# Kernel optimization log

Measured on AMD Instinct MI355X. Metric: run time of the kernel, lower is better.

Reference implementation:

```python
import jax, jax.numpy as jnp
import numpy as np

D_MODEL = 1024
N_HEAD = 16
HEAD_DIM = D_MODEL // N_HEAD

def setup_inputs() -> dict:
    key = jax.random.key(0)
    k1, k2, k3 = jax.random.split(key, 3)
    x = jax.random.normal(k1, (2, 2048, D_MODEL), dtype=jnp.float32)
    # torch Linear weights: [out_features, in_features]; scale like default init
    w_in = jax.random.normal(k2, (3 * D_MODEL, D_MODEL), dtype=jnp.float32) * (1.0 / np.sqrt(D_MODEL))
    w_out = jax.random.normal(k3, (D_MODEL, D_MODEL), dtype=jnp.float32) * (1.0 / np.sqrt(D_MODEL))
    return {"x": x, "w_in": w_in, "w_out": w_out}

def reference(x, w_in, w_out):
    B, T, D = x.shape
    qkv = jnp.einsum('btd,ed->bte', x, w_in)  # [B,T,3D]
    q, k, v = jnp.split(qkv, 3, axis=2)
    def heads(t):
        return t.reshape(B, T, N_HEAD, HEAD_DIM).transpose(0, 2, 1, 3)  # [B,H,T,hd]
    q, k, v = heads(q), heads(k), heads(v)
    att = jnp.einsum('bhqd,bhkd->bhqk', q, k) / np.sqrt(HEAD_DIM).astype(np.float32)
    # NOTE: original uses .tril() (zeroing, NOT -inf) before softmax — faithful reproduction
    causal = jnp.tril(jnp.ones((T, T), dtype=bool))
    att = jnp.where(causal, att, 0.0)
    att = jax.nn.softmax(att, axis=-1)
    out = jnp.einsum('bhqk,bhkd->bhqd', att, v)
    out = out.transpose(0, 2, 1, 3).reshape(B, T, D)
    return jnp.einsum('btd,ed->bte', out, w_out)
```

## Files before the change

### kernel.cpp

```cpp
#include <hip/hip_runtime.h>
#include <hip/hip_bf16.h>
#include <stdint.h>

#define TSEQ   2048
#define DMODEL 1024
#define NHEAD  16
#define HDIM   64

typedef __attribute__((ext_vector_type(8))) __bf16 bf16x8;
typedef __attribute__((ext_vector_type(4))) float f32x4;
typedef __attribute__((ext_vector_type(8))) unsigned short u16x8;

#define SC_LOG2E 0.18033688011112042f

#if __has_builtin(__builtin_amdgcn_exp2f)
#define EXP2F(x) __builtin_amdgcn_exp2f(x)
#else
#define EXP2F(x) __expf(0.6931471805599453f * (x))
#endif

__device__ __forceinline__ unsigned short f2bf(float f) {
    __hip_bfloat16 h = __float2bfloat16(f);
    return __builtin_bit_cast(unsigned short, h);
}
__device__ __forceinline__ float bf2f(unsigned short u) {
    union { unsigned int i; float f; } v;
    v.i = ((unsigned int)u) << 16;
    return v.f;
}

__device__ __forceinline__ void gld_lds16(const void* g, void* s) {
    __builtin_amdgcn_global_load_lds(
        (__attribute__((address_space(1))) void*)(void*)g,
        (__attribute__((address_space(3))) void*)s, 16, 0, 0);
}

#define NX4  (4096 * 1024 / 4)
#define NWI4 (3072 * 1024 / 4)
#define NWO4 (1024 * 1024 / 4)
__global__ void cast3_kernel(const float* __restrict__ x,
                             const float* __restrict__ wi,
                             const float* __restrict__ wo,
                             unsigned short* __restrict__ ox,
                             unsigned short* __restrict__ owi,
                             unsigned short* __restrict__ owo) {
    int i = blockIdx.x * blockDim.x + threadIdx.x;
    const float* s;
    unsigned short* d;
    int off;
    if (i < NX4)              { s = x;  d = ox;  off = i; }
    else if (i < NX4 + NWI4)  { s = wi; d = owi; off = i - NX4; }
    else                      { s = wo; d = owo; off = i - NX4 - NWI4; }
    float4 v = ((const float4*)s)[off];
    ushort4 u;
    u.x = f2bf(v.x); u.y = f2bf(v.y); u.z = f2bf(v.z); u.w = f2bf(v.w);
    ((ushort4*)d)[off] = u;
}

template<bool STORE_F32>
__global__ __launch_bounds__(256, 2)
void gemm_bt(const unsigned short* __restrict__ A,
             const unsigned short* __restrict__ B,
             void* __restrict__ C, int M, int N, int K) {
    (void)M;
    __shared__ unsigned short As[128 * 32];
    __shared__ unsigned short Bs[128 * 32];
    const int tid = threadIdx.x;
    const int nb = N >> 7;
    const int bm = blockIdx.x / nb;
    const int bn = blockIdx.x % nb;
    const int w  = tid >> 6, l = tid & 63;
    const int wr = w >> 1,  wc = w & 1;
    const int lr = l & 15,  lg = l >> 4;

    f32x4 acc[4][4] = {};

    const unsigned short* Ab = A + (size_t)bm * 128 * K;
    const unsigned short* Bb = B + (size_t)bn * 128 * K;

    const int c0 = tid, c1 = tid + 256;
    const int ar0 = c0 >> 2, ak0 = (c0 & 3) * 8;
    const int ar1 = c1 >> 2, ak1 = (c1 & 3) * 8;

    for (int kt = 0; kt < K; kt += 32) {
        __syncthreads();
        gld_lds16(Ab + (size_t)ar0 * K + kt + ak0, As + c0 * 8);
        gld_lds16(Ab + (size_t)ar1 * K + kt + ak1, As + c1 * 8);
        gld_lds16(Bb + (size_t)ar0 * K + kt + ak0, Bs + c0 * 8);
        gld_lds16(Bb + (size_t)ar1 * K + kt + ak1, Bs + c1 * 8);
        __syncthreads();

        bf16x8 af[4], bfr[4];
#pragma unroll
        for (int i = 0; i < 4; i++)
            af[i] = *(const bf16x8*)(As + (wr * 64 + i * 16 + lr) * 32 + lg * 8);
#pragma unroll
        for (int i = 0; i < 4; i++)
            bfr[i] = *(const bf16x8*)(Bs + (wc * 64 + i * 16 + lr) * 32 + lg * 8);
#pragma unroll
        for (int mi = 0; mi < 4; mi++)
#pragma unroll
            for (int ni = 0; ni < 4; ni++)
                acc[mi][ni] = __builtin_amdgcn_mfma_f32_16x16x32_bf16(
                    af[mi], bfr[ni], acc[mi][ni], 0, 0, 0);
    }

    const int row0 = bm * 128 + wr * 64;
    const int col0 = bn * 128 + wc * 64;
    const float qsc = (!STORE_F32 && bn < 8) ? SC_LOG2E : 1.0f;
#pragma unroll
    for (int mi = 0; mi < 4; mi++)
#pragma unroll
        for (int ni = 0; ni < 4; ni++)
#pragma unroll
            for (int r = 0; r < 4; r++) {
                const int row = row0 + mi * 16 + lg * 4 + r;
                const int col = col0 + ni * 16 + lr;
                if (STORE_F32)
                    ((float*)C)[(size_t)row * N + col] = acc[mi][ni][r];
                else
                    ((unsigned short*)C)[(size_t)row * N + col] =
                        f2bf(acc[mi][ni][r] * qsc);
            }
}

__global__ __launch_bounds__(256)
void vtran_kernel(const unsigned short* __restrict__ qkv,
                  unsigned short* __restrict__ vtg,
                  float* __restrict__ ts) {
    __shared__ unsigned short T[64][72];
    const int bid = blockIdx.x;
    const int kb_ = bid & 31;
    const int bh  = bid >> 5;
    const int b = bh >> 4, h = bh & 15;
    const int tid = threadIdx.x;

    const int r = tid >> 2, cq = (tid & 3) * 16;
    const unsigned short* src =
        qkv + ((size_t)(b * TSEQ + kb_ * 64 + r)) * 3072 + 2048 + h * 64 + cq;
    u16x8 v0 = *(const u16x8*)src;
    u16x8 v1 = *(const u16x8*)(src + 8);
#pragma unroll
    for (int i = 0; i < 8; i++) T[r][cq + i] = v0[i];
#pragma unroll
    for (int i = 0; i < 8; i++) T[r][cq + 8 + i] = v1[i];
    __syncthreads();

    const int d = tid >> 2, kq = (tid & 3) * 16;
    u16x8 o0, o1;
#pragma unroll
    for (int i = 0; i < 8; i++) o0[i] = T[kq + i][d];
#pragma unroll
    for (int i = 0; i < 8; i++) o1[i] = T[kq + 8 + i][d];
    unsigned short* dst = vtg + ((size_t)bh * 64 + d) * TSEQ + kb_ * 64 + kq;
    *(u16x8*)dst = o0;
    *(u16x8*)(dst + 8) = o1;

    float ps = 0.f;
#pragma unroll
    for (int i = 0; i < 8; i++) ps += bf2f(o0[i]) + bf2f(o1[i]);
    ps += __shfl_xor(ps, 1);
    ps += __shfl_xor(ps, 2);
    if ((tid & 3) == 0)
        ts[((size_t)bh * 32 + kb_) * 64 + d] = ps;
}

__global__ void vsuf2_kernel(const float* __restrict__ ts,
                             float* __restrict__ tsuf) {
    const int bh = blockIdx.x, d = threadIdx.x;
    float acc = 0.f;
    for (int t = 31; t >= 0; --t) {
        tsuf[((size_t)bh * 32 + t) * 64 + d] = acc;
        acc += ts[((size_t)bh * 32 + t) * 64 + d];
    }
}

__global__ __launch_bounds__(256, 2)
void attn_kernel(const unsigned short* __restrict__ qkv,
                 const unsigned short* __restrict__ vtg,
                 const float* __restrict__ tsuf,
                 unsigned short* __restrict__ out) {
    __shared__ __attribute__((aligned(16))) unsigned short Ks[2][4096];
    __shared__ __attribute__((aligned(16))) unsigned short Vs[2][4096];
    __shared__ __attribute__((aligned(16))) unsigned short Pl[4][32 * 72];

    const int tid = threadIdx.x;
    const int w = tid >> 6, l = tid & 63, lr = l & 15, lg = l >> 4;
    const int bid = blockIdx.x;
    const int j  = bid >> 5;
    const int s  = (j < 8) ? j : 23 - j;
    const int bh = (bid & 7) * 4 + ((bid >> 3) & 3);
    const int b = bh >> 4, h = bh & 15;
    const int strip  = 2 * s + ((w < 2) ? 1 : 0);
    const int lastkt = strip;
    const int ntiles = 2 * s + 2;
    const size_t rowbase = (size_t)b * TSEQ;
    const int qrow0 = strip * 64 + (w & 1) * 32;

    bf16x8 qf[2][2];
#pragma unroll
    for (int mi = 0; mi < 2; mi++) {
        const unsigned short* qp =
            qkv + (rowbase + qrow0 + mi * 16 + lr) * 3072 + h * 64 + lg * 8;
        qf[mi][0] = *(const bf16x8*)qp;
        qf[mi][1] = *(const bf16x8*)(qp + 32);
    }

    bf16x8 onesf;
#pragma unroll
    for (int i = 0; i < 8; i++) onesf[i] = (__bf16)1.0f;

    const unsigned short* ksrc[2];
    const unsigned short* vsrc[2];
#pragma unroll
    for (int jj = 0; jj < 2; jj++) {
        const int d = tid + jj * 256;
        const int fr = (d >> 7) * 16 + (d & 15);
        const int cc = ((d >> 6) & 1) * 32 + ((d & 63) >> 4) * 8;
        ksrc[jj] = qkv + (rowbase + fr) * 3072 + 1024 + h * 64 + cc;
        vsrc[jj] = vtg + ((size_t)bh * 64 + fr) * TSEQ + cc;
    }

#define STAGE(kt_, bufi) do {                                      \
        const size_t ko_ = (size_t)(kt_) * 64 * 3072;              \
        const int vo_ = (kt_) * 64;                                \
        gld_lds16(ksrc[0] + ko_, &Ks[bufi][tid * 8]);              \
        gld_lds16(ksrc[1] + ko_, &Ks[bufi][tid * 8 + 2048]);       \
        gld_lds16(vsrc[0] + vo_, &Vs[bufi][tid * 8]);              \
        gld_lds16(vsrc[1] + vo_, &Vs[bufi][tid * 8 + 2048]);       \
    } while (0)

    f32x4 o[2][4] = {};
    f32x4 rs[2] = {};
    unsigned short* pw = &Pl[w][0];

    STAGE(0, 0);
    __syncthreads();

    int cur = 0;
    for (int kt = 0; kt < ntiles; ++kt) {
        if (kt + 1 < ntiles) STAGE(kt + 1, cur ^ 1);

        if (kt <= lastkt) {
            const unsigned short* kc = Ks[cur];
            const unsigned short* vc = Vs[cur];

            bf16x8 kb[4][2];
#pragma unroll
            for (int f = 0; f < 4; f++) {
                kb[f][0] = *(const bf16x8*)(kc + ((f * 2 + 0) * 64 + l) * 8);
                kb[f][1] = *(const bf16x8*)(kc + ((f * 2 + 1) * 64 + l) * 8);
            }

            float pvv[2][4][4];
            __builtin_amdgcn_s_setprio(1);
#pragma unroll
            for (int mi = 0; mi < 2; mi++)
#pragma unroll
                for (int f = 0; f < 4; f++) {
                    f32x4 z = {0.f, 0.f, 0.f, 0.f};
                    f32x4 sv = __builtin_amdgcn_mfma_f32_16x16x32_bf16(qf[mi][0], kb[f][0], z, 0, 0, 0);
                    sv = __builtin_amdgcn_mfma_f32_16x16x32_bf16(qf[mi][1], kb[f][1], sv, 0, 0, 0);
#pragma unroll
                    for (int r = 0; r < 4; r++) pvv[mi][f][r] = sv[r];
                }
            __builtin_amdgcn_s_setprio(0);

            if (kt == lastkt) {
#pragma unroll
                for (int mi = 0; mi < 2; mi++)
#pragma unroll
                    for (int f = 0; f < 4; f++) {
                        const int kcol = kt * 64 + f * 16 + lr;
#pragma unroll
                        for (int r = 0; r < 4; r++) {
                            const int qr = qrow0 + mi * 16 + lg * 4 + r;
                            if (kcol > qr) pvv[mi][f][r] = 0.f;
                        }
                    }
            }

#pragma unroll
            for (int mi = 0; mi < 2; mi++)
#pragma unroll
                for (int f = 0; f < 4; f++)
#pragma unroll
                    for (int r = 0; r < 4; r++) {
                        float pp = EXP2F(pvv[mi][f][r]);
                        pw[(mi * 16 + lg * 4 + r) * 72 + f * 16 + lr] = f2bf(pp);
                    }

            bf16x8 pa[2][2];
#pragma unroll
            for (int mi = 0; mi < 2; mi++) {
                pa[mi][0] = *(const bf16x8*)(pw + (mi * 16 + lr) * 72 + lg * 8);
                pa[mi][1] = *(const bf16x8*)(pw + (mi * 16 + lr) * 72 + 32 + lg * 8);
            }
            bf16x8 vb[4][2];
#pragma unroll
            for (int f2 = 0; f2 < 4; f2++) {
                vb[f2][0] = *(const bf16x8*)(vc + ((f2 * 2 + 0) * 64 + l) * 8);
                vb[f2][1] = *(const bf16x8*)(vc + ((f2 * 2 + 1) * 64 + l) * 8);
            }
            __builtin_amdgcn_s_setprio(1);
#pragma unroll
            for (int mi = 0; mi < 2; mi++) {
                rs[mi] = __builtin_amdgcn_mfma_f32_16x16x32_bf16(pa[mi][0], onesf, rs[mi], 0, 0, 0);
                rs[mi] = __builtin_amdgcn_mfma_f32_16x16x32_bf16(pa[mi][1], onesf, rs[mi], 0, 0, 0);
#pragma unroll
                for (int f2 = 0; f2 < 4; f2++) {
                    o[mi][f2] = __builtin_amdgcn_mfma_f32_16x16x32_bf16(pa[mi][0], vb[f2][0], o[mi][f2], 0, 0, 0);
                    o[mi][f2] = __builtin_amdgcn_mfma_f32_16x16x32_bf16(pa[mi][1], vb[f2][1], o[mi][f2], 0, 0, 0);
                }
            }
            __builtin_amdgcn_s_setprio(0);
        }

        __syncthreads();
        cur ^= 1;
    }
#undef STAGE

    const float nmask = (float)((31 - lastkt) * 64);
    const float* tp = tsuf + ((size_t)bh * 32 + lastkt) * 64;
#pragma unroll
    for (int mi = 0; mi < 2; mi++)
#pragma unroll
        for (int r = 0; r < 4; r++) {
            const float inv = 1.f / (rs[mi][r] + nmask);
#pragma unroll
            for (int f2 = 0; f2 < 4; f2++) {
                float num = o[mi][f2][r] + tp[f2 * 16 + lr];
                out[(rowbase + qrow0 + mi * 16 + lg * 4 + r) * 1024 + h * 64 + f2 * 16 + lr] =
                    f2bf(num * inv);
            }
        }
}

extern "C" void kernel_launch(void* const* d_in, const int* in_sizes, int n_in,
                              void* d_out, int out_size, void* d_ws, size_t ws_size,
                              hipStream_t stream) {
    const float* x     = (const float*)d_in[0];
    const float* w_in  = (const float*)d_in[1];
    const float* w_out = (const float*)d_in[2];

    unsigned short* ws  = (unsigned short*)d_ws;
    unsigned short* xb  = ws;
    unsigned short* wib = xb  + (size_t)4096 * 1024;
    unsigned short* wob = wib + (size_t)3072 * 1024;
    unsigned short* qkv = wob + (size_t)1024 * 1024;
    unsigned short* ao  = qkv + (size_t)4096 * 3072;
    float* tsuf = (float*)(ao + (size_t)4096 * 1024);
    unsigned short* vtg = (unsigned short*)(tsuf + 32 * 32 * 64);
    float* ts = (float*)(vtg + (size_t)32 * 64 * 2048);

    cast3_kernel<<<(NX4 + NWI4 + NWO4) / 256, 256, 0, stream>>>(
        x, w_in, w_out, xb, wib, wob);

    gemm_bt<false><<<(4096 / 128) * (3072 / 128), 256, 0, stream>>>(
        xb, wib, qkv, 4096, 3072, 1024);
    vtran_kernel<<<32 * 32, 256, 0, stream>>>(qkv, vtg, ts);
    vsuf2_kernel<<<32, 64, 0, stream>>>(ts, tsuf);
    attn_kernel<<<512, 256, 0, stream>>>(qkv, vtg, tsuf, ao);
    gemm_bt<true><<<(4096 / 128) * (1024 / 128), 256, 0, stream>>>(
        ao, wob, (float*)d_out, 4096, 1024, 1024);
}
```

Baseline: 116.4 us.

## Fold suffix-sum kernel into attention, compute row sums in VALU, transpose QK MFMA

```diff
diff --git a/kernel.cpp b/kernel.cpp
--- a/kernel.cpp
+++ b/kernel.cpp
@@ -27,6 +27,11 @@
     union { unsigned int i; float f; } v;
     v.i = ((unsigned int)u) << 16;
     return v.f;
+}
+__device__ __forceinline__ unsigned int cvtpk_bf16(float lo, float hi) {
+    unsigned int r;
+    asm("v_cvt_pk_bf16_f32 %0, %1, %2" : "=v"(r) : "v"(lo), "v"(hi));
+    return r;
 }
 
 __device__ __forceinline__ void gld_lds16(const void* g, void* s) {
@@ -58,7 +63,7 @@
 }
 
 template<bool STORE_F32>
-__global__ __launch_bounds__(256, 2)
+__global__ __launch_bounds__(256, 3)
 void gemm_bt(const unsigned short* __restrict__ A,
              const unsigned short* __restrict__ B,
              void* __restrict__ C, int M, int N, int K) {
@@ -165,20 +170,10 @@
         ts[((size_t)bh * 32 + kb_) * 64 + d] = ps;
 }
 
-__global__ void vsuf2_kernel(const float* __restrict__ ts,
-                             float* __restrict__ tsuf) {
-    const int bh = blockIdx.x, d = threadIdx.x;
-    float acc = 0.f;
-    for (int t = 31; t >= 0; --t) {
-        tsuf[((size_t)bh * 32 + t) * 64 + d] = acc;
-        acc += ts[((size_t)bh * 32 + t) * 64 + d];
-    }
-}
-
 __global__ __launch_bounds__(256, 2)
 void attn_kernel(const unsigned short* __restrict__ qkv,
                  const unsigned short* __restrict__ vtg,
-                 const float* __restrict__ tsuf,
+                 const float* __restrict__ ts,
                  unsigned short* __restrict__ out) {
     __shared__ __attribute__((aligned(16))) unsigned short Ks[2][4096];
     __shared__ __attribute__((aligned(16))) unsigned short Vs[2][4096];
@@ -206,10 +201,6 @@
         qf[mi][1] = *(const bf16x8*)(qp + 32);
     }
 
-    bf16x8 onesf;
-#pragma unroll
-    for (int i = 0; i < 8; i++) onesf[i] = (__bf16)1.0f;
-
     const unsigned short* ksrc[2];
     const unsigned short* vsrc[2];
 #pragma unroll
@@ -231,7 +222,7 @@
     } while (0)
 
     f32x4 o[2][4] = {};
-    f32x4 rs[2] = {};
+    float ps[2] = {0.f, 0.f};
     unsigned short* pw = &Pl[w][0];
 
     STAGE(0, 0);
@@ -259,8 +250,8 @@
 #pragma unroll
                 for (int f = 0; f < 4; f++) {
                     f32x4 z = {0.f, 0.f, 0.f, 0.f};
-                    f32x4 sv = __builtin_amdgcn_mfma_f32_16x16x32_bf16(qf[mi][0], kb[f][0], z, 0, 0, 0);
-                    sv = __builtin_amdgcn_mfma_f32_16x16x32_bf16(qf[mi][1], kb[f][1], sv, 0, 0, 0);
+                    f32x4 sv = __builtin_amdgcn_mfma_f32_16x16x32_bf16(kb[f][0], qf[mi][0], z, 0, 0, 0);
+                    sv = __builtin_amdgcn_mfma_f32_16x16x32_bf16(kb[f][1], qf[mi][1], sv, 0, 0, 0);
 #pragma unroll
                     for (int r = 0; r < 4; r++) pvv[mi][f][r] = sv[r];
                 }
@@ -268,27 +259,32 @@
 
             if (kt == lastkt) {
 #pragma unroll
-                for (int mi = 0; mi < 2; mi++)
-#pragma unroll
-                    for (int f = 0; f < 4; f++) {
-                        const int kcol = kt * 64 + f * 16 + lr;
+                for (int mi = 0; mi < 2; mi++) {
+                    const int qr = qrow0 + mi * 16 + lr;
+#pragma unroll
+                    for (int f = 0; f < 4; f++)
 #pragma unroll
                         for (int r = 0; r < 4; r++) {
-                            const int qr = qrow0 + mi * 16 + lg * 4 + r;
+                            const int kcol = kt * 64 + f * 16 + lg * 4 + r;
                             if (kcol > qr) pvv[mi][f][r] = 0.f;
                         }
-                    }
+                }
             }
 
 #pragma unroll
             for (int mi = 0; mi < 2; mi++)
 #pragma unroll
-                for (int f = 0; f < 4; f++)
-#pragma unroll
-                    for (int r = 0; r < 4; r++) {
-                        float pp = EXP2F(pvv[mi][f][r]);
-                        pw[(mi * 16 + lg * 4 + r) * 72 + f * 16 + lr] = f2bf(pp);
-                    }
+                for (int f = 0; f < 4; f++) {
+                    float p0 = EXP2F(pvv[mi][f][0]);
+                    float p1 = EXP2F(pvv[mi][f][1]);
+                    float p2 = EXP2F(pvv[mi][f][2]);
+                    float p3 = EXP2F(pvv[mi][f][3]);
+                    ps[mi] += (p0 + p1) + (p2 + p3);
+                    uint2 pk;
+                    pk.x = cvtpk_bf16(p0, p1);
+                    pk.y = cvtpk_bf16(p2, p3);
+                    *(uint2*)(pw + (mi * 16 + lr) * 72 + f * 16 + lg * 4) = pk;
+                }
 
             bf16x8 pa[2][2];
 #pragma unroll
@@ -304,15 +300,12 @@
             }
             __builtin_amdgcn_s_setprio(1);
 #pragma unroll
-            for (int mi = 0; mi < 2; mi++) {
-                rs[mi] = __builtin_amdgcn_mfma_f32_16x16x32_bf16(pa[mi][0], onesf, rs[mi], 0, 0, 0);
-                rs[mi] = __builtin_amdgcn_mfma_f32_16x16x32_bf16(pa[mi][1], onesf, rs[mi], 0, 0, 0);
+            for (int mi = 0; mi < 2; mi++)
 #pragma unroll
                 for (int f2 = 0; f2 < 4; f2++) {
                     o[mi][f2] = __builtin_amdgcn_mfma_f32_16x16x32_bf16(pa[mi][0], vb[f2][0], o[mi][f2], 0, 0, 0);
                     o[mi][f2] = __builtin_amdgcn_mfma_f32_16x16x32_bf16(pa[mi][1], vb[f2][1], o[mi][f2], 0, 0, 0);
                 }
-            }
             __builtin_amdgcn_s_setprio(0);
         }
 
@@ -321,16 +314,34 @@
     }
 #undef STAGE
 
+#pragma unroll
+    for (int mi = 0; mi < 2; mi++) {
+        ps[mi] += __shfl_xor(ps[mi], 16);
+        ps[mi] += __shfl_xor(ps[mi], 32);
+    }
+    float rget[2][4];
+#pragma unroll
+    for (int mi = 0; mi < 2; mi++)
+#pragma unroll
+        for (int r = 0; r < 4; r++)
+            rget[mi][r] = __shfl(ps[mi], lg * 4 + r);
+
+    float tpv[4] = {0.f, 0.f, 0.f, 0.f};
+    for (int t = lastkt + 1; t < 32; ++t) {
+        const float* tsp = ts + ((size_t)bh * 32 + t) * 64 + lr;
+#pragma unroll
+        for (int f2 = 0; f2 < 4; f2++) tpv[f2] += tsp[f2 * 16];
+    }
+
     const float nmask = (float)((31 - lastkt) * 64);
-    const float* tp = tsuf + ((size_t)bh * 32 + lastkt) * 64;
 #pragma unroll
     for (int mi = 0; mi < 2; mi++)
 #pragma unroll
         for (int r = 0; r < 4; r++) {
-            const float inv = 1.f / (rs[mi][r] + nmask);
+            const float inv = 1.f / (rget[mi][r] + nmask);
 #pragma unroll
             for (int f2 = 0; f2 < 4; f2++) {
-                float num = o[mi][f2][r] + tp[f2 * 16 + lr];
+                float num = o[mi][f2][r] + tpv[f2];
                 out[(rowbase + qrow0 + mi * 16 + lg * 4 + r) * 1024 + h * 64 + f2 * 16 + lr] =
                     f2bf(num * inv);
             }
@@ -350,18 +361,16 @@
     unsigned short* wob = wib + (size_t)3072 * 1024;
     unsigned short* qkv = wob + (size_t)1024 * 1024;
     unsigned short* ao  = qkv + (size_t)4096 * 3072;
-    float* tsuf = (float*)(ao + (size_t)4096 * 1024);
-    unsigned short* vtg = (unsigned short*)(tsuf + 32 * 32 * 64);
-    float* ts = (float*)(vtg + (size_t)32 * 64 * 2048);
+    float* tsbuf = (float*)(ao + (size_t)4096 * 1024);
+    unsigned short* vtg = (unsigned short*)(tsbuf + 32 * 32 * 64);
 
     cast3_kernel<<<(NX4 + NWI4 + NWO4) / 256, 256, 0, stream>>>(
         x, w_in, w_out, xb, wib, wob);
 
     gemm_bt<false><<<(4096 / 128) * (3072 / 128), 256, 0, stream>>>(
         xb, wib, qkv, 4096, 3072, 1024);
-    vtran_kernel<<<32 * 32, 256, 0, stream>>>(qkv, vtg, ts);
-    vsuf2_kernel<<<32, 64, 0, stream>>>(ts, tsuf);
-    attn_kernel<<<512, 256, 0, stream>>>(qkv, vtg, tsuf, ao);
+    vtran_kernel<<<32 * 32, 256, 0, stream>>>(qkv, vtg, tsbuf);
+    attn_kernel<<<512, 256, 0, stream>>>(qkv, vtg, tsbuf, ao);
     gemm_bt<true><<<(4096 / 128) * (1024 / 128), 256, 0, stream>>>(
         ao, wob, (float*)d_out, 4096, 1024, 1024);
 }
```

Result: faster. 113.6 us (-2.4%).
